# Performance work log

Hardware: AMD Instinct MI355X
Metric: run time of the kernel (lower is better)

## Reference

```python
import jax, jax.numpy as jnp
import numpy as np

DIM = 768
H = 12
HEAD = DIM // H
SCALE = HEAD ** -0.5
NMM, NV, NA = 8, 4, 4


def _cross_attn(x1, x2, qw, kvw, pw, pb):
    # x1: [B,N1,C] queries, x2: [B,N2,C] keys/values. Weights stored [in,out].
    B, N1, C = x1.shape
    N2 = x2.shape[1]
    q = (x1 @ qw).reshape(B, N1, H, HEAD).transpose(0, 2, 1, 3)        # [B,H,N1,d]
    kv = (x2 @ kvw).reshape(B, N2, 2, H, HEAD)
    k = kv[:, :, 0].transpose(0, 2, 1, 3)                               # [B,H,N2,d]
    v = kv[:, :, 1].transpose(0, 2, 1, 3)
    attn = jax.nn.softmax(jnp.einsum('bhnd,bhmd->bhnm', q, k) * SCALE, axis=-1)
    o = jnp.einsum('bhnm,bhmd->bhnd', attn, v).transpose(0, 2, 1, 3).reshape(B, N1, C)
    return o @ pw + pb, attn


def setup_inputs() -> dict:
    key = jax.random.key(0)
    ks = jax.random.split(key, 16)
    s = 0.02
    inp = {
        'xmm': jax.random.normal(ks[0], (64, 16, DIM), jnp.float32),
        'xv': jax.random.normal(ks[1], (64, 784, DIM), jnp.float32),
        'xa': jax.random.normal(ks[2], (64, 512, DIM), jnp.float32),
        # visual cross-attn params (weights stored [in,out] = torch W.T)
        'qv_w': s * jax.random.normal(ks[3], (DIM, DIM), jnp.float32),
        'kvv_w': s * jax.random.normal(ks[4], (DIM, 2 * DIM), jnp.float32),
        'projv_w': s * jax.random.normal(ks[5], (DIM, DIM), jnp.float32),
        'projv_b': jnp.zeros((DIM,), jnp.float32),
        # audio cross-attn params
        'qa_w': s * jax.random.normal(ks[6], (DIM, DIM), jnp.float32),
        'kva_w': s * jax.random.normal(ks[7], (DIM, 2 * DIM), jnp.float32),
        'proja_w': s * jax.random.normal(ks[8], (DIM, DIM), jnp.float32),
        'proja_b': jnp.zeros((DIM,), jnp.float32),
        # factorized fusion attention params (dim_ratio=1.0 -> inner dim = DIM)
        'fq_w': s * jax.random.normal(ks[9], (DIM, DIM), jnp.float32),
        'fk_w': s * jax.random.normal(ks[10], (2 * DIM, DIM), jnp.float32),
        'fv_w': s * jax.random.normal(ks[11], (2 * DIM, DIM), jnp.float32),
        'fproj_w': s * jax.random.normal(ks[12], (DIM, DIM), jnp.float32),
        'fproj_b': jnp.zeros((DIM,), jnp.float32),
    }
    return inp


def reference(xmm, xv, xa, qv_w, kvv_w, projv_w, projv_b,
              qa_w, kva_w, proja_w, proja_b,
              fq_w, fk_w, fv_w, fproj_w, fproj_b):
    B = xmm.shape[0]
    xmm2 = xmm[:, :NMM]
    xmm_v, _ = _cross_attn(xmm[:, NMM:NMM + NV], xv, qv_w, kvv_w, projv_w, projv_b)
    xmm_a, _ = _cross_attn(xmm[:, NMM + NV:], xa, qa_w, kva_w, proja_w, proja_b)
    # outer-product token fusion: [B, NV*NA, 2*DIM]
    xva = jnp.concatenate([
        jnp.broadcast_to(xmm_v[:, :, None, :], (B, NV, NA, DIM)),
        jnp.broadcast_to(xmm_a[:, None, :, :], (B, NV, NA, DIM)),
    ], axis=-1).reshape(B, NV * NA, 2 * DIM)
    q = (xmm2 @ fq_w).reshape(B, NMM, H, -1).transpose(0, 2, 1, 3)
    k = (xva @ fk_w).reshape(B, NV * NA, H, -1).transpose(0, 2, 1, 3)
    v = (xva @ fv_w).reshape(B, NV * NA, H, -1).transpose(0, 2, 1, 3)
    attn = jax.nn.softmax(jnp.einsum('bhnd,bhmd->bhnm', q, k) * SCALE, axis=-1)
    o = jnp.einsum('bhnm,bhmd->bhnd', attn, v).transpose(0, 2, 1, 3).reshape(B, NMM, DIM)
    o = o @ fproj_w + fproj_b
    xmm_out = jnp.concatenate([o, xmm_v, xmm_a], axis=1)  # [B,16,DIM]
    return xmm_out, attn
```

## Files before the change

### kernel.cpp

```cpp
#include <hip/hip_runtime.h>
#include <stdint.h>

typedef unsigned short u16;
typedef unsigned int u32;
typedef __attribute__((ext_vector_type(8))) short short8;
typedef __attribute__((ext_vector_type(4))) float floatx4;


__device__ __forceinline__ u16 f2bf_rne(float f) {
  u32 u = __float_as_uint(f);
  return (u16)((u + 0x7fffu + ((u >> 16) & 1u)) >> 16);
}
__device__ __forceinline__ u32 pack_rne_u(u32 a, u32 b) {
  a += 0x7fffu + ((a >> 16) & 1u);
  b += 0x7fffu + ((b >> 16) & 1u);
  return __builtin_amdgcn_perm(b, a, 0x07060302u);
}
__device__ __forceinline__ short8 pack8(uint4 a, uint4 b) {
  union { u32 u[4]; short8 s; } cv;
  cv.u[0] = pack_rne_u(a.x, a.y);
  cv.u[1] = pack_rne_u(a.z, a.w);
  cv.u[2] = pack_rne_u(b.x, b.y);
  cv.u[3] = pack_rne_u(b.z, b.w);
  return cv.s;
}

__device__ __forceinline__ void block_sync_lds() {
  asm volatile("s_waitcnt lgkmcnt(0)" ::: "memory");
  __builtin_amdgcn_s_barrier();
  asm volatile("" ::: "memory");
}

__device__ __forceinline__ void sg_body(
    float (*sAt)[20], float (*sW)[64],
    const float* __restrict__ A, int a_pitch, int a_rb, int a_off,
    const float* __restrict__ W, const float* __restrict__ bias,
    float* __restrict__ Cout, int c_pitch, int c_rb, int c_off,
    int rt, int n0)
{
  const int t = threadIdx.x;
  const int g = t >> 6;
  const int c = t & 63;

  float acc[4] = {0.f, 0.f, 0.f, 0.f};

  for (int ks = 0; ks < 12; ++ks) {
    {
      int r = t >> 4;
      int c4 = (t & 15) * 4;
      int lr = rt * 16 + r;
      int grow = (lr / a_rb) * a_pitch + a_off + (lr % a_rb);
      float4 v = *(const float4*)(A + (size_t)grow * 768 + ks * 64 + c4);
      sAt[c4 + 0][r] = v.x;
      sAt[c4 + 1][r] = v.y;
      sAt[c4 + 2][r] = v.z;
      sAt[c4 + 3][r] = v.w;
    }
#pragma unroll
    for (int u = 0; u < 4; ++u) {
      int unit = t + u * 256;
      int r = unit >> 4;
      int c4 = (unit & 15) * 4;
      *(float4*)&sW[r][c4] = *(const float4*)(W + (size_t)(ks * 64 + r) * 768 + n0 + c4);
    }
    __syncthreads();
#pragma unroll 8
    for (int k = 0; k < 64; ++k) {
      float4 a4 = *(const float4*)&sAt[k][g * 4];
      float w = sW[k][c];
      acc[0] += a4.x * w;
      acc[1] += a4.y * w;
      acc[2] += a4.z * w;
      acc[3] += a4.w * w;
    }
    __syncthreads();
  }

  float bs = bias ? bias[n0 + c] : 0.f;
#pragma unroll
  for (int rr = 0; rr < 4; ++rr) {
    int lr = rt * 16 + g * 4 + rr;
    int grow = (lr / c_rb) * c_pitch + c_off + (lr % c_rb);
    Cout[(size_t)grow * 768 + n0 + c] = acc[rr] + bs;
  }
}

__global__ __launch_bounds__(256) void qproj(
    const float* __restrict__ xmm,
    const float* __restrict__ qv_w, const float* __restrict__ qa_w,
    const float* __restrict__ fq_w,
    float* __restrict__ q_v, float* __restrict__ q_a, float* __restrict__ q_f)
{
  __shared__ float sAt[64][20];
  __shared__ float sW[64][64];
  int rt = blockIdx.x;
  int n0 = blockIdx.y * 64;
  if (rt < 16)
    sg_body(sAt, sW, xmm, 16, 4, 8, qv_w, nullptr, q_v, 4, 4, 0, rt, n0);
  else if (rt < 32)
    sg_body(sAt, sW, xmm, 16, 4, 12, qa_w, nullptr, q_a, 4, 4, 0, rt - 16, n0);
  else
    sg_body(sAt, sW, xmm, 16, 8, 0, fq_w, nullptr, q_f, 8, 8, 0, rt - 32, n0);
}

__global__ __launch_bounds__(256) void proj2(
    const float* __restrict__ o_v, const float* __restrict__ o_a,
    const float* __restrict__ projv_w, const float* __restrict__ projv_b,
    const float* __restrict__ proja_w, const float* __restrict__ proja_b,
    float* __restrict__ out0)
{
  __shared__ float sAt[64][20];
  __shared__ float sW[64][64];
  int z = blockIdx.z;
  sg_body(sAt, sW, z ? o_a : o_v, 4, 4, 0,
          z ? proja_w : projv_w, z ? proja_b : projv_b,
          out0, 16, 4, z ? 12 : 8, blockIdx.x, blockIdx.y * 64);
}

__global__ __launch_bounds__(256) void fkv(
    const float* __restrict__ out0,
    const float* __restrict__ fk_w, const float* __restrict__ fv_w,
    float* __restrict__ kbase)
{
  __shared__ float sAt[64][20];
  __shared__ float sW[64][64];
  int z = blockIdx.z;
  const float* W = (z < 2) ? (fk_w + (size_t)(z & 1) * 768 * 768)
                           : (fv_w + (size_t)(z & 1) * 768 * 768);
  int a_off = (z & 1) ? 12 : 8;
  sg_body(sAt, sW, out0, 16, 4, a_off, W, nullptr,
          kbase + (size_t)z * 256 * 768, 4, 4, 0, blockIdx.x, blockIdx.y * 64);
}

__global__ __launch_bounds__(256) void fproj(
    const float* __restrict__ o_f,
    const float* __restrict__ fproj_w, const float* __restrict__ fproj_b,
    float* __restrict__ out0)
{
  __shared__ float sAt[64][20];
  __shared__ float sW[64][64];
  sg_body(sAt, sW, o_f, 8, 8, 0, fproj_w, fproj_b, out0, 16, 8, 0,
          blockIdx.x, blockIdx.y * 64);
}

__global__ __launch_bounds__(256) void qtilde(
    const float* __restrict__ q_v, const float* __restrict__ q_a,
    const float* __restrict__ kvv_w, const float* __restrict__ kva_w,
    u16* __restrict__ Qt_v, u16* __restrict__ Qt_a)
{
  __shared__ float sAt[64][20];
  __shared__ float sW[64][65];

  const int rt = blockIdx.x;
  const int nt = blockIdx.y;
  const int path = blockIdx.z / 12;
  const int h = blockIdx.z % 12;
  const float* q = path ? q_a : q_v;
  const float* kvw = path ? kva_w : kvv_w;
  u16* Qt = path ? Qt_a : Qt_v;

  const int t = threadIdx.x;
  const int g = t >> 6;
  const int c = t & 63;
  const int n0 = nt * 64;

  {
    int r = t >> 4;
    int c4 = (t & 15) * 4;
    float4 v = *(const float4*)(q + (size_t)(rt * 16 + r) * 768 + h * 64 + c4);
    sAt[c4 + 0][r] = v.x;
    sAt[c4 + 1][r] = v.y;
    sAt[c4 + 2][r] = v.z;
    sAt[c4 + 3][r] = v.w;
  }
#pragma unroll
  for (int u = 0; u < 4; ++u) {
    int unit = t + u * 256;
    int d = unit >> 4;
    int c4 = (unit & 15) * 4;
    float4 v = *(const float4*)(kvw + (size_t)(n0 + d) * 1536 + h * 64 + c4);
    sW[d][c4 + 0] = v.x;
    sW[d][c4 + 1] = v.y;
    sW[d][c4 + 2] = v.z;
    sW[d][c4 + 3] = v.w;
  }
  __syncthreads();

  float acc[4] = {0.f, 0.f, 0.f, 0.f};
#pragma unroll 16
  for (int e = 0; e < 64; ++e) {
    float4 a4 = *(const float4*)&sAt[e][g * 4];
    float w = sW[c][e];
    acc[0] += a4.x * w;
    acc[1] += a4.y * w;
    acc[2] += a4.z * w;
    acc[3] += a4.w * w;
  }
#pragma unroll
  for (int rr = 0; rr < 4; ++rr) {
    int rl = rt * 16 + g * 4 + rr;
    Qt[((size_t)(rl >> 2) * 48 + h * 4 + (rl & 3)) * 768 + n0 + c] = f2bf_rne(acc[rr]);
  }
}

__global__ __launch_bounds__(256) void attn_logits(
    const u16* __restrict__ Qt_v, const u16* __restrict__ Qt_a,
    const float* __restrict__ Xv, const float* __restrict__ Xa,
    float* __restrict__ Sv, float* __restrict__ Sa)
{
  const int z = blockIdx.z;
  const int jt = blockIdx.x;
  if (z == 1 && jt >= 4) return;
  const u16* Qt = z ? Qt_a : Qt_v;
  const float* X = z ? Xa : Xv;
  float* S = z ? Sa : Sv;
  const int N2 = z ? 512 : 784;

  const int t = threadIdx.x;
  const int lane = t & 63;
  const int wave = t >> 6;
  const int b = blockIdx.y;
  const int j0 = jt * 128;
  const u16* Qb = Qt + (size_t)b * 48 * 768;
  const float* Xb = X + (size_t)b * N2 * 768;

  const int ql = lane & 15;
  const int qs = lane >> 4;

  int row0 = j0 + wave * 32 + ql;
  int row1 = row0 + 16;
  if (row0 > N2 - 1) row0 = N2 - 1;
  if (row1 > N2 - 1) row1 = N2 - 1;
  const float* xP0 = Xb + (size_t)row0 * 768 + qs * 8;
  const float* xP1 = Xb + (size_t)row1 * 768 + qs * 8;
  const u16* qP0 = Qb + (size_t)(0 * 16 + ql) * 768 + qs * 8;
  const u16* qP1 = Qb + (size_t)(1 * 16 + ql) * 768 + qs * 8;
  const u16* qP2 = Qb + (size_t)(2 * 16 + ql) * 768 + qs * 8;

  floatx4 acc[3][2];
#pragma unroll
  for (int i = 0; i < 3; ++i)
#pragma unroll
    for (int j = 0; j < 2; ++j) acc[i][j] = (floatx4){0.f, 0.f, 0.f, 0.f};

#pragma unroll 4
  for (int kk = 0; kk < 24; ++kk) {
    uint4 x0a = *(const uint4*)(xP0 + kk * 32);
    uint4 x0b = *(const uint4*)(xP0 + kk * 32 + 4);
    uint4 x1a = *(const uint4*)(xP1 + kk * 32);
    uint4 x1b = *(const uint4*)(xP1 + kk * 32 + 4);
    short8 qa0 = *(const short8*)(qP0 + kk * 32);
    short8 qa1 = *(const short8*)(qP1 + kk * 32);
    short8 qa2 = *(const short8*)(qP2 + kk * 32);
    short8 bf0 = pack8(x0a, x0b);
    short8 bf1 = pack8(x1a, x1b);
    acc[0][0] = __builtin_amdgcn_mfma_f32_16x16x32_bf16(qa0, bf0, acc[0][0], 0, 0, 0);
    acc[0][1] = __builtin_amdgcn_mfma_f32_16x16x32_bf16(qa0, bf1, acc[0][1], 0, 0, 0);
    acc[1][0] = __builtin_amdgcn_mfma_f32_16x16x32_bf16(qa1, bf0, acc[1][0], 0, 0, 0);
    acc[1][1] = __builtin_amdgcn_mfma_f32_16x16x32_bf16(qa1, bf1, acc[1][1], 0, 0, 0);
    acc[2][0] = __builtin_amdgcn_mfma_f32_16x16x32_bf16(qa2, bf0, acc[2][0], 0, 0, 0);
    acc[2][1] = __builtin_amdgcn_mfma_f32_16x16x32_bf16(qa2, bf1, acc[2][1], 0, 0, 0);
  }

  const int quad = lane >> 4;
  const int lc = lane & 15;
#pragma unroll
  for (int i = 0; i < 3; ++i)
#pragma unroll
    for (int jj = 0; jj < 2; ++jj) {
      int col = j0 + wave * 32 + jj * 16 + lc;
      if (col < N2) {
        int row0s = i * 16 + quad * 4;
#pragma unroll
        for (int r = 0; r < 4; ++r)
          S[((size_t)b * 48 + row0s + r) * N2 + col] = acc[i][jj][r] * 0.125f;
      }
    }
}

__global__ __launch_bounds__(256) void softmax_p(
    const float* __restrict__ Sv, const float* __restrict__ Sa,
    u16* __restrict__ Pv, u16* __restrict__ Pa)
{
  const int z = blockIdx.z;
  const float* S = z ? Sa : Sv;
  u16* P = z ? Pa : Pv;
  const int N2 = z ? 512 : 784;
  const int N2p = z ? 512 : 832;

  const int hh = blockIdx.x;
  const int b = blockIdx.y;
  const int t = threadIdx.x;
  const int lane = t & 63;
  const int wave = t >> 6;
  const int row = hh * 4 + wave;
  const float* Srow = S + ((size_t)b * 48 + row) * N2;
  u16* Prow = P + ((size_t)b * 48 + row) * N2p;

  float m = -1e30f;
  for (int j = lane; j < N2; j += 64) m = fmaxf(m, Srow[j]);
#pragma unroll
  for (int off = 32; off > 0; off >>= 1) m = fmaxf(m, __shfl_xor(m, off));

  float e[13];
  float l = 0.f;
  int cnt = 0;
  for (int j = lane; j < N2; j += 64) {
    float p = __expf(Srow[j] - m);
    e[cnt++] = p;
    l += p;
  }
#pragma unroll
  for (int off = 32; off > 0; off >>= 1) l += __shfl_xor(l, off);
  float inv = 1.0f / l;

  cnt = 0;
  for (int j = lane; j < N2; j += 64) Prow[j] = f2bf_rne(e[cnt++] * inv);
  for (int j = N2 + lane; j < N2p; j += 64) Prow[j] = 0;
}

__global__ __launch_bounds__(256) void attn_px(
    const u16* __restrict__ Pv, const u16* __restrict__ Pa,
    const float* __restrict__ Xv, const float* __restrict__ Xa,
    float* __restrict__ Ov, float* __restrict__ Oa)
{
  const int z = blockIdx.z;
  const u16* P = z ? Pa : Pv;
  const float* X = z ? Xa : Xv;
  float* O = z ? Oa : Ov;
  const int N2 = z ? 512 : 784;
  const int N2p = z ? 512 : 832;

  __shared__ __align__(16) u16 sXT[2][128 * 72];

  const int t = threadIdx.x;
  const int lane = t & 63;
  const int wave = t >> 6;
  const int nt = blockIdx.x;
  const int b = blockIdx.y;
  const int n0 = nt * 128;
  const u16* Pb = P + (size_t)b * 48 * N2p;
  const float* Xb = X + (size_t)b * N2 * 768;
  const int Ks = N2p >> 6;

  const int jp0 = t >> 5;
  const int nq4 = (t & 31) * 4;
  const int qrow0 = lane & 15;
  const int qcb = (lane >> 4) * 8;

  floatx4 acc[3][2];
#pragma unroll
  for (int i = 0; i < 3; ++i)
#pragma unroll
    for (int j = 0; j < 2; ++j) acc[i][j] = (floatx4){0.f, 0.f, 0.f, 0.f};

  uint4 xA[4][2], xB[4][2];
  short8 qr[3][2];

#define PX_LOADX(dst, ks_)                                                     \
  do {                                                                         \
    _Pragma("unroll") for (int u = 0; u < 4; ++u) {                            \
      int j_ = (ks_) * 64 + (jp0 + u * 8) * 2;                                 \
      uint4 a0_ = {0u, 0u, 0u, 0u}, a1_ = {0u, 0u, 0u, 0u};                    \
      if (j_ < N2)                                                             \
        a0_ = *(const uint4*)(Xb + (size_t)j_ * 768 + n0 + nq4);               \
      if (j_ + 1 < N2)                                                         \
        a1_ = *(const uint4*)(Xb + (size_t)(j_ + 1) * 768 + n0 + nq4);         \
      dst[u][0] = a0_;                                                         \
      dst[u][1] = a1_;                                                         \
    }                                                                          \
  } while (0)

#define PX_LOADP(ks_)                                                          \
  do {                                                                         \
    _Pragma("unroll") for (int i = 0; i < 3; ++i)                              \
      _Pragma("unroll") for (int kk = 0; kk < 2; ++kk)                         \
        qr[i][kk] = *(const short8*)(Pb + (size_t)(i * 16 + qrow0) * N2p +     \
                                     (ks_) * 64 + kk * 32 + qcb);              \
  } while (0)

#define PX_WRITEX(src, bufp)                                                   \
  do {                                                                         \
    _Pragma("unroll") for (int u = 0; u < 4; ++u) {                            \
      int jl_ = (jp0 + u * 8) * 2;                                             \
      u32 w0_ = pack_rne_u(src[u][0].x, src[u][1].x);                          \
      u32 w1_ = pack_rne_u(src[u][0].y, src[u][1].y);                          \
      u32 w2_ = pack_rne_u(src[u][0].z, src[u][1].z);                          \
      u32 w3_ = pack_rne_u(src[u][0].w, src[u][1].w);                          \
      _Pragma("unroll") for (int m_ = 0; m_ < 4; ++m_) {                       \
        int n_ = nq4 + m_;                                                     \
        int sw_ = (((n_ >> 2) & 7) ^ ((n_ & 3) << 1)) * 8;                     \
        u32 wv_ = (m_ == 0) ? w0_ : (m_ == 1) ? w1_ : (m_ == 2) ? w2_ : w3_;   \
        *(u32*)((bufp) + n_ * 72 + (jl_ ^ sw_)) = wv_;                         \
      }                                                                        \
    }                                                                          \
  } while (0)

#define PX_COMPUTE(bufp)                                                       \
  do {                                                                         \
    _Pragma("unroll") for (int kk = 0; kk < 2; ++kk) {                         \
      _Pragma("unroll") for (int jj = 0; jj < 2; ++jj) {                       \
        int n_ = wave * 32 + jj * 16 + qrow0;                                  \
        int sw_ = (((n_ >> 2) & 7) ^ ((n_ & 3) << 1)) * 8;                     \
        int kb_ = kk * 32 + qcb;                                               \
        short8 bfr_ = *(const short8*)((bufp) + n_ * 72 + (kb_ ^ sw_));        \
        _Pragma("unroll") for (int i = 0; i < 3; ++i)                          \
          acc[i][jj] = __builtin_amdgcn_mfma_f32_16x16x32_bf16(                \
              qr[i][kk], bfr_, acc[i][jj], 0, 0, 0);                           \
      }                                                                        \
    }                                                                          \
  } while (0)

  u16* sT0 = &sXT[0][0];
  u16* sT1 = &sXT[1][0];

  PX_LOADX(xA, 0);
  PX_LOADP(0);
  int ks = 0;
  for (;;) {
    int more0 = (ks + 1 < Ks);
    if (more0) PX_LOADX(xB, ks + 1);
    PX_WRITEX(xA, sT0);
    block_sync_lds();
    PX_COMPUTE(sT0);
    if (!more0) break;
    PX_LOADP(ks + 1);
    ++ks;
    int more1 = (ks + 1 < Ks);
    if (more1) PX_LOADX(xA, ks + 1);
    PX_WRITEX(xB, sT1);
    block_sync_lds();
    PX_COMPUTE(sT1);
    if (!more1) break;
    PX_LOADP(ks + 1);
    ++ks;
  }
#undef PX_LOADX
#undef PX_LOADP
#undef PX_WRITEX
#undef PX_COMPUTE

  const int quad = lane >> 4;
  const int lc = lane & 15;
#pragma unroll
  for (int i = 0; i < 3; ++i)
#pragma unroll
    for (int jj = 0; jj < 2; ++jj) {
      int col = n0 + wave * 32 + jj * 16 + lc;
      int row0 = i * 16 + quad * 4;
#pragma unroll
      for (int r = 0; r < 4; ++r)
        O[((size_t)b * 48 + row0 + r) * 768 + col] = acc[i][jj][r];
    }
}

__global__ __launch_bounds__(256) void omix(
    const float* __restrict__ O_v, const float* __restrict__ O_a,
    const float* __restrict__ kvv_w, const float* __restrict__ kva_w,
    float* __restrict__ o_v, float* __restrict__ o_a)
{
  __shared__ float sAt[64][20];
  __shared__ float sW[64][64];

  const int z = blockIdx.z;
  const float* Ob = z ? O_a : O_v;
  const float* kvw = z ? kva_w : kvv_w;
  float* oo = z ? o_a : o_v;

  const int rt = blockIdx.x;
  const int h = blockIdx.y;
  const int t = threadIdx.x;
  const int g = t >> 6;
  const int c = t & 63;

  float acc[4] = {0.f, 0.f, 0.f, 0.f};

  for (int ks = 0; ks < 12; ++ks) {
    {
      int r = t >> 4;
      int c4 = (t & 15) * 4;
      int rl = rt * 16 + r;
      int arow = (rl >> 2) * 48 + h * 4 + (rl & 3);
      float4 v = *(const float4*)(Ob + (size_t)arow * 768 + ks * 64 + c4);
      sAt[c4 + 0][r] = v.x;
      sAt[c4 + 1][r] = v.y;
      sAt[c4 + 2][r] = v.z;
      sAt[c4 + 3][r] = v.w;
    }
#pragma unroll
    for (int u = 0; u < 4; ++u) {
      int unit = t + u * 256;
      int k = unit >> 4;
      int c4 = (unit & 15) * 4;
      *(float4*)&sW[k][c4] = *(const float4*)(kvw + (size_t)(ks * 64 + k) * 1536 + 768 + h * 64 + c4);
    }
    __syncthreads();
#pragma unroll 8
    for (int k = 0; k < 64; ++k) {
      float4 a4 = *(const float4*)&sAt[k][g * 4];
      float w = sW[k][c];
      acc[0] += a4.x * w;
      acc[1] += a4.y * w;
      acc[2] += a4.z * w;
      acc[3] += a4.w * w;
    }
    __syncthreads();
  }

#pragma unroll
  for (int rr = 0; rr < 4; ++rr) {
    int rl = rt * 16 + g * 4 + rr;
    oo[(size_t)rl * 768 + h * 64 + c] = acc[rr];
  }
}

__global__ __launch_bounds__(256) void fusion_attn(
    const float* __restrict__ Qf,
    const float* __restrict__ K1, const float* __restrict__ K2,
    const float* __restrict__ V1, const float* __restrict__ V2,
    float* __restrict__ Of,
    float* __restrict__ AttnOut)
{
  const int h = blockIdx.x;
  const int b = blockIdx.y;
  const int t = threadIdx.x;
  const int lane = t & 63;
  const int wave = t >> 6;

  __shared__ float sQ[8][64];
  __shared__ float sK1[4][64], sK2[4][64], sV1[4][64], sV2[4][64];
  __shared__ float sP[8][16];

  for (int idx = t; idx < 512; idx += 256)
    sQ[idx >> 6][idx & 63] = Qf[((size_t)(b * 8 + (idx >> 6))) * 768 + h * 64 + (idx & 63)];
  {
    size_t base = ((size_t)(b * 4 + wave)) * 768 + h * 64 + lane;
    sK1[wave][lane] = K1[base];
    sK2[wave][lane] = K2[base];
    sV1[wave][lane] = V1[base];
    sV2[wave][lane] = V2[base];
  }
  __syncthreads();

  if (t < 128) {
    int qi = t >> 4, m = t & 15, iv = m >> 2, ja = m & 3;
    float s = 0.f;
#pragma unroll
    for (int d = 0; d < 64; ++d) s += sQ[qi][d] * (sK1[iv][d] + sK2[ja][d]);
    s *= 0.125f;
    float mx = s;
#pragma unroll
    for (int off = 8; off > 0; off >>= 1) mx = fmaxf(mx, __shfl_xor(mx, off, 16));
    float p = __expf(s - mx);
    float l = p;
#pragma unroll
    for (int off = 8; off > 0; off >>= 1) l += __shfl_xor(l, off, 16);
    p = p / l;
    sP[qi][m] = p;
    AttnOut[(((size_t)b * 12 + h) * 8 + qi) * 16 + m] = p;
  }
  __syncthreads();

  for (int idx = t; idx < 512; idx += 256) {
    int qi = idx >> 6, d = idx & 63;
    float o = 0.f;
#pragma unroll
    for (int m = 0; m < 16; ++m) o += sP[qi][m] * (sV1[m >> 2][d] + sV2[m & 3][d]);
    Of[((size_t)(b * 8 + qi)) * 768 + h * 64 + d] = o;
  }
}

extern "C" void kernel_launch(void* const* d_in, const int* in_sizes, int n_in,
                              void* d_out, int out_size, void* d_ws, size_t ws_size,
                              hipStream_t stream)
{
  const float* xmm     = (const float*)d_in[0];
  const float* xv      = (const float*)d_in[1];
  const float* xa      = (const float*)d_in[2];
  const float* qv_w    = (const float*)d_in[3];
  const float* kvv_w   = (const float*)d_in[4];
  const float* projv_w = (const float*)d_in[5];
  const float* projv_b = (const float*)d_in[6];
  const float* qa_w    = (const float*)d_in[7];
  const float* kva_w   = (const float*)d_in[8];
  const float* proja_w = (const float*)d_in[9];
  const float* proja_b = (const float*)d_in[10];
  const float* fq_w    = (const float*)d_in[11];
  const float* fk_w    = (const float*)d_in[12];
  const float* fv_w    = (const float*)d_in[13];
  const float* fproj_w = (const float*)d_in[14];
  const float* fproj_b = (const float*)d_in[15];

  float* out0 = (float*)d_out;
  float* out1 = out0 + (size_t)64 * 16 * 768;

  char* ws = (char*)d_ws;
  size_t off = 0;
  float* q_v  = (float*)(ws + off); off += (size_t)256 * 768 * 4;
  float* q_a  = (float*)(ws + off); off += (size_t)256 * 768 * 4;
  float* q_f  = (float*)(ws + off); off += (size_t)512 * 768 * 4;
  u16*   Qt_v = (u16*)(ws + off);   off += (size_t)64 * 48 * 768 * 2;
  u16*   Qt_a = (u16*)(ws + off);   off += (size_t)64 * 48 * 768 * 2;
  float* S_v  = (float*)(ws + off); off += (size_t)64 * 48 * 784 * 4;
  float* S_a  = (float*)(ws + off); off += (size_t)64 * 48 * 512 * 4;
  u16*   P_v  = (u16*)(ws + off);   off += (size_t)64 * 48 * 832 * 2;
  u16*   P_a  = (u16*)(ws + off);   off += (size_t)64 * 48 * 512 * 2;
  float* O_v  = (float*)(ws + off); off += (size_t)64 * 48 * 768 * 4;
  float* O_a  = (float*)(ws + off); off += (size_t)64 * 48 * 768 * 4;
  float* o_v  = (float*)(ws + off); off += (size_t)256 * 768 * 4;
  float* o_a  = (float*)(ws + off); off += (size_t)256 * 768 * 4;
  float* kbase = (float*)(ws + off); off += (size_t)4 * 256 * 768 * 4;
  float* o_f  = (float*)(ws + off); off += (size_t)512 * 768 * 4;

  float* k1 = kbase;
  float* k2 = kbase + (size_t)256 * 768;
  float* v1 = kbase + (size_t)2 * 256 * 768;
  float* v2 = kbase + (size_t)3 * 256 * 768;

  qproj<<<dim3(64, 12), 256, 0, stream>>>(xmm, qv_w, qa_w, fq_w, q_v, q_a, q_f);
  qtilde<<<dim3(16, 12, 24), 256, 0, stream>>>(q_v, q_a, kvv_w, kva_w, Qt_v, Qt_a);
  attn_logits<<<dim3(7, 64, 2), 256, 0, stream>>>(Qt_v, Qt_a, xv, xa, S_v, S_a);
  softmax_p<<<dim3(12, 64, 2), 256, 0, stream>>>(S_v, S_a, P_v, P_a);
  attn_px<<<dim3(6, 64, 2), 256, 0, stream>>>(P_v, P_a, xv, xa, O_v, O_a);
  omix<<<dim3(16, 12, 2), 256, 0, stream>>>(O_v, O_a, kvv_w, kva_w, o_v, o_a);
  proj2<<<dim3(16, 12, 2), 256, 0, stream>>>(o_v, o_a, projv_w, projv_b, proja_w, proja_b, out0);
  fkv<<<dim3(16, 12, 4), 256, 0, stream>>>(out0, fk_w, fv_w, kbase);
  fusion_attn<<<dim3(12, 64), 256, 0, stream>>>(q_f, k1, k2, v1, v2, o_f, out1);
  fproj<<<dim3(32, 12), 256, 0, stream>>>(o_f, fproj_w, fproj_b, out0);
}
```

Measured before the change: 608.2 us.

## Software-pipeline attn_logits global loads with explicit 4-deep prefetch via inline asm

Rewrites the attn_logits K-loop to issue global_load_dwordx4 through inline asm with SGPR base plus VGPR offset, keeping four iterations of X and Q loads in flight and waiting on vmcnt counters before each MFMA step. It also sets a launch bound of two blocks per CU. The aim is to hide global memory latency in a kernel that streams fp32 X from HBM. The cost is higher register pressure (28 uint4 buffers), and the hand-placed waitcnt and sched_barrier are fragile because the compiler may not track the asm loads.

```diff
diff --git a/kernel.cpp b/kernel.cpp
--- a/kernel.cpp
+++ b/kernel.cpp
@@ -23,6 +23,11 @@
   cv.u[2] = pack_rne_u(b.x, b.y);
   cv.u[3] = pack_rne_u(b.z, b.w);
   return cv.s;
+}
+__device__ __forceinline__ short8 as_s8(uint4 v) {
+  union { uint4 u; short8 s; } c;
+  c.u = v;
+  return c.s;
 }
 
 __device__ __forceinline__ void block_sync_lds() {
@@ -203,7 +208,7 @@
   }
 }
 
-__global__ __launch_bounds__(256) void attn_logits(
+__global__ __launch_bounds__(256, 2) void attn_logits(
     const u16* __restrict__ Qt_v, const u16* __restrict__ Qt_a,
     const float* __restrict__ Xv, const float* __restrict__ Xa,
     float* __restrict__ Sv, float* __restrict__ Sa)
@@ -221,8 +226,8 @@
   const int wave = t >> 6;
   const int b = blockIdx.y;
   const int j0 = jt * 128;
-  const u16* Qb = Qt + (size_t)b * 48 * 768;
-  const float* Xb = X + (size_t)b * N2 * 768;
+  const char* Qb8 = (const char*)(Qt + (size_t)b * 48 * 768);
+  const char* Xb8 = (const char*)(X + (size_t)b * N2 * 768);
 
   const int ql = lane & 15;
   const int qs = lane >> 4;
@@ -231,11 +236,11 @@
   int row1 = row0 + 16;
   if (row0 > N2 - 1) row0 = N2 - 1;
   if (row1 > N2 - 1) row1 = N2 - 1;
-  const float* xP0 = Xb + (size_t)row0 * 768 + qs * 8;
-  const float* xP1 = Xb + (size_t)row1 * 768 + qs * 8;
-  const u16* qP0 = Qb + (size_t)(0 * 16 + ql) * 768 + qs * 8;
-  const u16* qP1 = Qb + (size_t)(1 * 16 + ql) * 768 + qs * 8;
-  const u16* qP2 = Qb + (size_t)(2 * 16 + ql) * 768 + qs * 8;
+  const u32 voffX0 = (u32)(row0 * 3072 + qs * 32);
+  const u32 voffX1 = (u32)(row1 * 3072 + qs * 32);
+  const u32 voffQ0 = (u32)((0 * 16 + ql) * 1536 + qs * 16);
+  const u32 voffQ1 = (u32)((1 * 16 + ql) * 1536 + qs * 16);
+  const u32 voffQ2 = (u32)((2 * 16 + ql) * 1536 + qs * 16);
 
   floatx4 acc[3][2];
 #pragma unroll
@@ -243,24 +248,57 @@
 #pragma unroll
     for (int j = 0; j < 2; ++j) acc[i][j] = (floatx4){0.f, 0.f, 0.f, 0.f};
 
-#pragma unroll 4
-  for (int kk = 0; kk < 24; ++kk) {
-    uint4 x0a = *(const uint4*)(xP0 + kk * 32);
-    uint4 x0b = *(const uint4*)(xP0 + kk * 32 + 4);
-    uint4 x1a = *(const uint4*)(xP1 + kk * 32);
-    uint4 x1b = *(const uint4*)(xP1 + kk * 32 + 4);
-    short8 qa0 = *(const short8*)(qP0 + kk * 32);
-    short8 qa1 = *(const short8*)(qP1 + kk * 32);
-    short8 qa2 = *(const short8*)(qP2 + kk * 32);
-    short8 bf0 = pack8(x0a, x0b);
-    short8 bf1 = pack8(x1a, x1b);
-    acc[0][0] = __builtin_amdgcn_mfma_f32_16x16x32_bf16(qa0, bf0, acc[0][0], 0, 0, 0);
-    acc[0][1] = __builtin_amdgcn_mfma_f32_16x16x32_bf16(qa0, bf1, acc[0][1], 0, 0, 0);
-    acc[1][0] = __builtin_amdgcn_mfma_f32_16x16x32_bf16(qa1, bf0, acc[1][0], 0, 0, 0);
-    acc[1][1] = __builtin_amdgcn_mfma_f32_16x16x32_bf16(qa1, bf1, acc[1][1], 0, 0, 0);
-    acc[2][0] = __builtin_amdgcn_mfma_f32_16x16x32_bf16(qa2, bf0, acc[2][0], 0, 0, 0);
-    acc[2][1] = __builtin_amdgcn_mfma_f32_16x16x32_bf16(qa2, bf1, acc[2][1], 0, 0, 0);
-  }
+  uint4 xr[4][4];
+  uint4 qu[4][3];
+
+#define AL5_GL(DST, VOFF, BASE, IMM)                                           \
+  asm volatile("global_load_dwordx4 %0, %1, %2 offset:%3"                      \
+               : "=v"(DST) : "v"(VOFF), "s"(BASE), "n"(IMM));
+
+#define AL5_ISSUE(K)                                                           \
+  do {                                                                         \
+    AL5_GL(xr[(K) & 3][0], voffX0, Xb8, (K) * 128)                             \
+    AL5_GL(xr[(K) & 3][1], voffX0, Xb8, (K) * 128 + 16)                        \
+    AL5_GL(xr[(K) & 3][2], voffX1, Xb8, (K) * 128)                             \
+    AL5_GL(xr[(K) & 3][3], voffX1, Xb8, (K) * 128 + 16)                        \
+    AL5_GL(qu[(K) & 3][0], voffQ0, Qb8, (K) * 64)                              \
+    AL5_GL(qu[(K) & 3][1], voffQ1, Qb8, (K) * 64)                              \
+    AL5_GL(qu[(K) & 3][2], voffQ2, Qb8, (K) * 64)                              \
+  } while (0)
+
+#define AL5_STEP(K, W)                                                         \
+  do {                                                                         \
+    asm volatile("s_waitcnt vmcnt(%0)" :: "n"(W));                             \
+    __builtin_amdgcn_sched_barrier(0);                                         \
+    short8 bf0 = pack8(xr[(K) & 3][0], xr[(K) & 3][1]);                        \
+    short8 bf1 = pack8(xr[(K) & 3][2], xr[(K) & 3][3]);                        \
+    short8 q0 = as_s8(qu[(K) & 3][0]);                                         \
+    short8 q1 = as_s8(qu[(K) & 3][1]);                                         \
+    short8 q2 = as_s8(qu[(K) & 3][2]);                                         \
+    acc[0][0] = __builtin_amdgcn_mfma_f32_16x16x32_bf16(q0, bf0, acc[0][0], 0, 0, 0); \
+    acc[0][1] = __builtin_amdgcn_mfma_f32_16x16x32_bf16(q0, bf1, acc[0][1], 0, 0, 0); \
+    acc[1][0] = __builtin_amdgcn_mfma_f32_16x16x32_bf16(q1, bf0, acc[1][0], 0, 0, 0); \
+    acc[1][1] = __builtin_amdgcn_mfma_f32_16x16x32_bf16(q1, bf1, acc[1][1], 0, 0, 0); \
+    acc[2][0] = __builtin_amdgcn_mfma_f32_16x16x32_bf16(q2, bf0, acc[2][0], 0, 0, 0); \
+    acc[2][1] = __builtin_amdgcn_mfma_f32_16x16x32_bf16(q2, bf1, acc[2][1], 0, 0, 0); \
+    if ((K) + 4 < 24) AL5_ISSUE((K) + 4);                                      \
+  } while (0)
+
+  AL5_ISSUE(0);
+  AL5_ISSUE(1);
+  AL5_ISSUE(2);
+  AL5_ISSUE(3);
+
+  AL5_STEP(0, 21);  AL5_STEP(1, 21);  AL5_STEP(2, 21);  AL5_STEP(3, 21);
+  AL5_STEP(4, 21);  AL5_STEP(5, 21);  AL5_STEP(6, 21);  AL5_STEP(7, 21);
+  AL5_STEP(8, 21);  AL5_STEP(9, 21);  AL5_STEP(10, 21); AL5_STEP(11, 21);
+  AL5_STEP(12, 21); AL5_STEP(13, 21); AL5_STEP(14, 21); AL5_STEP(15, 21);
+  AL5_STEP(16, 21); AL5_STEP(17, 21); AL5_STEP(18, 21); AL5_STEP(19, 21);
+  AL5_STEP(20, 21); AL5_STEP(21, 14); AL5_STEP(22, 7);  AL5_STEP(23, 0);
+
+#undef AL5_GL
+#undef AL5_ISSUE
+#undef AL5_STEP
 
   const int quad = lane >> 4;
   const int lc = lane & 15;
```

After: 592.4 us. -2.6%, faster.
